# Kernel tuning notes

Hardware: AMD Instinct MI355X
Metric: run time of the kernel (lower is better)

Reference implementation:

```python
import jax, jax.numpy as jnp
import numpy as np

NL, NK = 10000, 2000          # ligand / keypoint node counts
ELL, EKL = 320000, 160000     # lig->lig and kp->lig edge counts
IN, HID, OUT = 128, 128, 128  # in_size, hidden_size, out_size
FDIM = 2 * IN + 1             # edge MLP input: [h_src, h_dst, dij]


def silu(x):
    return x * jax.nn.sigmoid(x)


def setup_inputs() -> dict:
    keys = iter(jax.random.split(jax.random.key(0), 64))

    def nrm(shape, scale=0.02):
        return jax.random.normal(next(keys), shape, dtype=jnp.float32) * scale

    d = {}
    d["h_lig"] = jax.random.normal(next(keys), (NL, IN), dtype=jnp.float32)
    d["h_kp"] = jax.random.normal(next(keys), (NK, IN), dtype=jnp.float32)
    d["x_lig"] = jax.random.normal(next(keys), (NL, 3), dtype=jnp.float32)
    d["x_kp"] = jax.random.normal(next(keys), (NK, 3), dtype=jnp.float32)
    # per-node normalizer (e.g. neighbor count); keep >= 1 to avoid blowup
    d["z_lig"] = jax.random.uniform(next(keys), (NL, 1), dtype=jnp.float32, minval=1.0, maxval=32.0)
    for e in ("ll", "kl"):
        d[e + "_eW1"] = nrm((FDIM, HID)); d[e + "_eb1"] = jnp.zeros((HID,), jnp.float32)
        d[e + "_eW2"] = nrm((HID, HID)); d[e + "_eb2"] = jnp.zeros((HID,), jnp.float32)
        d[e + "_aW"] = nrm((HID, 1)); d[e + "_ab"] = jnp.zeros((1,), jnp.float32)
        d[e + "_cW1"] = nrm((FDIM, HID)); d[e + "_cb1"] = jnp.zeros((HID,), jnp.float32)
        d[e + "_cW2"] = nrm((HID, HID)); d[e + "_cb2"] = jnp.zeros((HID,), jnp.float32)
        d[e + "_cW3"] = nrm((HID, 1), scale=0.001)  # xavier gain=0.001 final coord layer
    d["n_W1"] = nrm((IN + HID, HID)); d["n_b1"] = jnp.zeros((HID,), jnp.float32)
    d["n_W2"] = nrm((HID, OUT)); d["n_b2"] = jnp.zeros((OUT,), jnp.float32)
    d["ll_src"] = jax.random.randint(next(keys), (ELL,), 0, NL, dtype=jnp.int32)
    d["ll_dst"] = jax.random.randint(next(keys), (ELL,), 0, NL, dtype=jnp.int32)
    d["kl_src"] = jax.random.randint(next(keys), (EKL,), 0, NK, dtype=jnp.int32)
    d["kl_dst"] = jax.random.randint(next(keys), (EKL,), 0, NL, dtype=jnp.int32)
    return d


def _edge_messages(hs, hd, xs, xd, eW1, eb1, eW2, eb2, aW, ab, cW1, cb1, cW2, cb2, cW3):
    x_diff = xs - xd                                     # fn.u_sub_v
    dij = jnp.linalg.norm(x_diff, axis=1, keepdims=True)  # [E,1]
    x_diff = x_diff / (dij + 1.0)
    f = jnp.concatenate([hs, hd, dij], axis=1)           # [E, 2*IN+1]
    m = silu(f @ eW1 + eb1)
    m = silu(m @ eW2 + eb2)
    msg_h = m * jax.nn.sigmoid(m @ aW + ab)              # soft attention gate
    c = silu(f @ cW1 + cb1)
    c = silu(c @ cW2 + cb2)
    msg_x = (c @ cW3) * x_diff                           # use_tanh=False path
    return msg_h, msg_x


def reference(h_lig, h_kp, x_lig, x_kp, z_lig,
              ll_eW1, ll_eb1, ll_eW2, ll_eb2, ll_aW, ll_ab,
              ll_cW1, ll_cb1, ll_cW2, ll_cb2, ll_cW3,
              kl_eW1, kl_eb1, kl_eW2, kl_eb2, kl_aW, kl_ab,
              kl_cW1, kl_cb1, kl_cW2, kl_cb2, kl_cW3,
              n_W1, n_b1, n_W2, n_b2,
              ll_src, ll_dst, kl_src, kl_dst):
    # lig -> lig edges
    mh_ll, mx_ll = _edge_messages(h_lig[ll_src], h_lig[ll_dst], x_lig[ll_src], x_lig[ll_dst],
                                  ll_eW1, ll_eb1, ll_eW2, ll_eb2, ll_aW, ll_ab,
                                  ll_cW1, ll_cb1, ll_cW2, ll_cb2, ll_cW3)
    # kp -> lig edges
    mh_kl, mx_kl = _edge_messages(h_kp[kl_src], h_lig[kl_dst], x_kp[kl_src], x_lig[kl_dst],
                                  kl_eW1, kl_eb1, kl_eW2, kl_eb2, kl_aW, kl_ab,
                                  kl_cW1, kl_cb1, kl_cW2, kl_cb2, kl_cW3)
    nl = h_lig.shape[0]
    # multi_update_all with cross_reducer='sum', then per-node normalization by z
    h_neigh = (jax.ops.segment_sum(mh_ll, ll_dst, num_segments=nl)
               + jax.ops.segment_sum(mh_kl, kl_dst, num_segments=nl)) / z_lig
    x_neigh = (jax.ops.segment_sum(mx_ll, ll_dst, num_segments=nl)
               + jax.ops.segment_sum(mx_kl, kl_dst, num_segments=nl)) / z_lig
    nin = jnp.concatenate([h_lig, h_neigh], axis=1)
    h_out = h_lig + (silu(nin @ n_W1 + n_b1) @ n_W2 + n_b2)  # norm=False -> Identity
    x_out = x_lig + x_neigh
    return (h_out, x_out)
```

## Files before the change

### kernel.cpp

```cpp
#include <hip/hip_runtime.h>
#include <math.h>

#define EPB  32
#define MSTR 136
#define FSTR 264

typedef __attribute__((ext_vector_type(8))) short short8;
typedef __attribute__((ext_vector_type(4))) float f32x4;

__device__ __forceinline__ unsigned short f2bf(float x) {
    unsigned int u = __float_as_uint(x);
    u += 0x7fffu + ((u >> 16) & 1u);
    return (unsigned short)(u >> 16);
}
__device__ __forceinline__ float bf2f(short v) {
    return __uint_as_float(((unsigned int)(unsigned short)v) << 16);
}
__device__ __forceinline__ float fsilu(float x) {
    return x * (1.0f / (1.0f + __expf(-x)));
}
__device__ __forceinline__ float fsigm(float x) {
    return 1.0f / (1.0f + __expf(-x));
}
__device__ __forceinline__ void atomAddF(float* p, float v) {
    unsafeAtomicAdd(p, v);
}

struct PrepArgs { const float* src[10]; };

__global__ __launch_bounds__(256) void prep_hist_kernel(PrepArgs pa, short* __restrict__ wsb,
                                                        const int* __restrict__ lld,
                                                        const int* __restrict__ kld,
                                                        int* __restrict__ hist) {
    int idx = blockIdx.x * 256 + threadIdx.x;
    if (idx < 245760) {
        int pair = idx / 49152;
        int rem  = idx - pair * 49152;
        int second = (rem >= 32768) ? 1 : 0;
        int mi = pair * 2 + second;
        int within = second ? (rem - 32768) : rem;
        int n, k, K;
        if (second) { K = 128; n = within >> 7; k = within & 127; }
        else        { K = 256; n = within >> 8; k = within & 255; }
        int dstoff = pair * 49152 + second * 32768;
        wsb[dstoff + n * K + k] = (short)f2bf(pa.src[mi][k * 128 + n]);
        return;
    }
    idx -= 245760;
    if (idx < 320000) { atomicAdd(&hist[lld[idx]], 1); return; }
    idx -= 320000;
    if (idx < 160000) atomicAdd(&hist[10000 + kld[idx]], 1);
}

__global__ __launch_bounds__(256) void scan_kernel(const int* __restrict__ hist,
                                                   int* __restrict__ cursor) {
    __shared__ int bins[10000];
    __shared__ int ps[256];
    const int b = blockIdx.x, t = threadIdx.x;
    const int* h = hist + b * 10000;
    int* cur = cursor + b * 10000;
    for (int i = t; i < 10000; i += 256) bins[i] = h[i];
    __syncthreads();
    const int base = t * 40;
    int s = 0;
#pragma unroll 8
    for (int i = 0; i < 40; i++) { int ii = base + i; if (ii < 10000) s += bins[ii]; }
    ps[t] = s;
    __syncthreads();
    for (int off = 1; off < 256; off <<= 1) {
        int v = (t >= off) ? ps[t - off] : 0;
        __syncthreads();
        ps[t] += v;
        __syncthreads();
    }
    int run = ps[t] - s;
    for (int i = 0; i < 40; i++) {
        int ii = base + i;
        if (ii < 10000) { int c = bins[ii]; bins[ii] = run; run += c; }
    }
    __syncthreads();
    for (int i = t; i < 10000; i += 256) cur[i] = bins[i];
}

struct ProjDesc { const float* A; const short* Bt; short* out; const float* bias;
                  int rows; int ktb; int co; int hasb; };
struct CArgs {
    const int *lls, *lld, *kls, *kld;
    int* cursor;
    int *ll_ssrc, *ll_sdst, *kl_ssrc, *kl_sdst;
    ProjDesc d[8];
};

__global__ __launch_bounds__(256) void scatter_proj_kernel(CArgs ca) {
    __shared__ __align__(16) short a_lds[64 * MSTR];
    const int t = threadIdx.x;
    if (blockIdx.x < 1875) {
        int i = blockIdx.x * 256 + t;
        if (i < 320000) {
            int d = ca.lld[i];
            int p = atomicAdd(&ca.cursor[d], 1);
            ca.ll_ssrc[p] = ca.lls[i]; ca.ll_sdst[p] = d;
        } else if (i < 480000) {
            int j = i - 320000;
            int d = ca.kld[j];
            int p = atomicAdd(&ca.cursor[10000 + d], 1);
            ca.kl_ssrc[p] = ca.kls[j]; ca.kl_sdst[p] = d;
        }
        return;
    }
    const int pb = blockIdx.x - 1875;
    const int di = pb / 157, tile = pb - di * 157;
    const ProjDesc pd = ca.d[di];
    if (tile * 64 >= pd.rows) return;
    {
        const int r = t >> 2, q = t & 3;
        const int node = tile * 64 + r;
        short* arow = a_lds + r * MSTR + q * 32;
        if (node < pd.rows) {
            const float* ap = pd.A + (size_t)node * 128 + q * 32;
#pragma unroll
            for (int i = 0; i < 4; i++) {
                float4 v0 = *(const float4*)(ap + i * 8);
                float4 v1 = *(const float4*)(ap + i * 8 + 4);
                short8 o;
                o[0] = (short)f2bf(v0.x); o[1] = (short)f2bf(v0.y);
                o[2] = (short)f2bf(v0.z); o[3] = (short)f2bf(v0.w);
                o[4] = (short)f2bf(v1.x); o[5] = (short)f2bf(v1.y);
                o[6] = (short)f2bf(v1.z); o[7] = (short)f2bf(v1.w);
                *(short8*)(arow + i * 8) = o;
            }
        } else {
            short8 z = {0, 0, 0, 0, 0, 0, 0, 0};
#pragma unroll
            for (int i = 0; i < 4; i++) *(short8*)(arow + i * 8) = z;
        }
    }
    __syncthreads();

    const int ln = t & 63, wv = t >> 6;
    const int lrow = ln & 15, quad = ln >> 4;
    const int c0 = wv * 32 + lrow, c1 = c0 + 16;

    short8 bf0[4], bf1[4];
#pragma unroll
    for (int kt = 0; kt < 4; kt++) {
        bf0[kt] = *(const short8*)(pd.Bt + c0 * 256 + (pd.ktb + kt) * 32 + quad * 8);
        bf1[kt] = *(const short8*)(pd.Bt + c1 * 256 + (pd.ktb + kt) * 32 + quad * 8);
    }
    const float bb0 = pd.hasb ? pd.bias[c0] : 0.0f;
    const float bb1 = pd.hasb ? pd.bias[c1] : 0.0f;
#pragma unroll
    for (int mt = 0; mt < 4; mt++) {
        short8 af[4];
#pragma unroll
        for (int kt = 0; kt < 4; kt++)
            af[kt] = *(const short8*)(&a_lds[(mt * 16 + lrow) * MSTR + kt * 32 + quad * 8]);
        f32x4 a0 = {0.f, 0.f, 0.f, 0.f}, a1 = {0.f, 0.f, 0.f, 0.f};
#pragma unroll
        for (int kt = 0; kt < 4; kt++) {
            a0 = __builtin_amdgcn_mfma_f32_16x16x32_bf16(af[kt], bf0[kt], a0, 0, 0, 0);
            a1 = __builtin_amdgcn_mfma_f32_16x16x32_bf16(af[kt], bf1[kt], a1, 0, 0, 0);
        }
#pragma unroll
        for (int r = 0; r < 4; r++) {
            const int node = tile * 64 + mt * 16 + quad * 4 + r;
            if (node < pd.rows) {
                pd.out[(size_t)node * 256 + pd.co + c0] = (short)f2bf(a0[r] + bb0);
                pd.out[(size_t)node * 256 + pd.co + c1] = (short)f2bf(a1[r] + bb1);
            }
        }
    }
}

struct EdgeSet {
    const short *Ps, *Pd;
    const float *xs, *xd;
    const int *esrc, *edst;
    const float *w256e, *w256c;
    const short *W2t, *cW2t;
    const float *b2e, *b2c;
    const float *aW, *ab, *cW3;
};
struct EdgePair { EdgeSet s[2]; int split; };

__global__ __launch_bounds__(256, 8) void edge_kernel(EdgePair ep,
                                                      float* __restrict__ hne,
                                                      float* __restrict__ xne)
{
    __shared__ __align__(16) char mbuf[EPB * MSTR * 4];
    __shared__ float sv_l[EPB];
    __shared__ float gate_l[EPB];
    __shared__ float xdf[3][EPB];
    __shared__ int   dstl[EPB];
    __shared__ float gp[4][EPB];

    short* mh = (short*)mbuf;
    short* mc = (short*)(mbuf + EPB * MSTR * 2);
    float* msg = (float*)mbuf;

    const int isKL = (blockIdx.x >= ep.split) ? 1 : 0;
    const EdgeSet P = ep.s[isKL];
    const int eb = (blockIdx.x - (isKL ? ep.split : 0)) * EPB;
    const int t = threadIdx.x;

    {
        const int e = t >> 3, q = t & 7;
        const int eid = eb + e;
        const int s = P.esrc[eid], d = P.edst[eid];
        float dx = P.xs[s * 3 + 0] - P.xd[d * 3 + 0];
        float dy = P.xs[s * 3 + 1] - P.xd[d * 3 + 1];
        float dz = P.xs[s * 3 + 2] - P.xd[d * 3 + 2];
        float dd = sqrtf(dx * dx + dy * dy + dz * dz);
        if (q == 0) {
            dstl[e] = d;
            float inv = 1.0f / (dd + 1.0f);
            xdf[0][e] = dx * inv; xdf[1][e] = dy * inv; xdf[2][e] = dz * inv;
        }
        const short* psrow = P.Ps + (size_t)s * 256 + q * 16;
        const short* pdrow = P.Pd + (size_t)d * 256 + q * 16;
#pragma unroll
        for (int path = 0; path < 2; path++) {
            const short* ps = psrow + path * 128;
            const short* pq = pdrow + path * 128;
            const float* wq = (path ? P.w256c : P.w256e) + q * 16;
            short* mrow = (path ? mc : mh) + e * MSTR + q * 16;
#pragma unroll
            for (int i = 0; i < 2; i++) {
                short8 a = *(const short8*)(ps + i * 8);
                short8 b = *(const short8*)(pq + i * 8);
                float4 wA = *(const float4*)(wq + i * 8);
                float4 wB = *(const float4*)(wq + i * 8 + 4);
                short8 o;
                o[0] = (short)f2bf(fsilu(bf2f(a[0]) + bf2f(b[0]) + dd * wA.x));
                o[1] = (short)f2bf(fsilu(bf2f(a[1]) + bf2f(b[1]) + dd * wA.y));
                o[2] = (short)f2bf(fsilu(bf2f(a[2]) + bf2f(b[2]) + dd * wA.z));
                o[3] = (short)f2bf(fsilu(bf2f(a[3]) + bf2f(b[3]) + dd * wA.w));
                o[4] = (short)f2bf(fsilu(bf2f(a[4]) + bf2f(b[4]) + dd * wB.x));
                o[5] = (short)f2bf(fsilu(bf2f(a[5]) + bf2f(b[5]) + dd * wB.y));
                o[6] = (short)f2bf(fsilu(bf2f(a[6]) + bf2f(b[6]) + dd * wB.z));
                o[7] = (short)f2bf(fsilu(bf2f(a[7]) + bf2f(b[7]) + dd * wB.w));
                *(short8*)(mrow + i * 8) = o;
            }
        }
    }
    __syncthreads();

    const int ln = t & 63, wv = t >> 6;
    const int lrow = ln & 15, quad = ln >> 4;
    const int c0 = wv * 32 + lrow, c1 = c0 + 16;

    {
        short8 bf0[4], bf1[4];
#pragma unroll
        for (int kt = 0; kt < 4; kt++) {
            bf0[kt] = *(const short8*)(P.cW2t + c0 * 128 + kt * 32 + quad * 8);
            bf1[kt] = *(const short8*)(P.cW2t + c1 * 128 + kt * 32 + quad * 8);
        }
        const float cw0 = P.cW3[c0], cw1 = P.cW3[c1];
        const float bb0 = P.b2c[c0], bb1 = P.b2c[c1];
#pragma unroll
        for (int mt = 0; mt < 2; mt++) {
            short8 af[4];
#pragma unroll
            for (int kt = 0; kt < 4; kt++)
                af[kt] = *(const short8*)(&mc[(mt * 16 + lrow) * MSTR + kt * 32 + quad * 8]);
            f32x4 a0 = {0.f, 0.f, 0.f, 0.f}, a1 = {0.f, 0.f, 0.f, 0.f};
#pragma unroll
            for (int kt = 0; kt < 4; kt++) {
                a0 = __builtin_amdgcn_mfma_f32_16x16x32_bf16(af[kt], bf0[kt], a0, 0, 0, 0);
                a1 = __builtin_amdgcn_mfma_f32_16x16x32_bf16(af[kt], bf1[kt], a1, 0, 0, 0);
            }
#pragma unroll
            for (int r = 0; r < 4; r++) {
                float v0 = fsilu(a0[r] + bb0);
                float v1 = fsilu(a1[r] + bb1);
                float g = v0 * cw0 + v1 * cw1;
                g += __shfl_xor(g, 1, 64);
                g += __shfl_xor(g, 2, 64);
                g += __shfl_xor(g, 4, 64);
                g += __shfl_xor(g, 8, 64);
                if (lrow == 0) gp[wv][mt * 16 + quad * 4 + r] = g;
            }
        }
    }
    __syncthreads();
    if (t < EPB) sv_l[t] = gp[0][t] + gp[1][t] + gp[2][t] + gp[3][t];
    __syncthreads();

    float m2s[2][8];
    {
        short8 bf0[4], bf1[4];
#pragma unroll
        for (int kt = 0; kt < 4; kt++) {
            bf0[kt] = *(const short8*)(P.W2t + c0 * 128 + kt * 32 + quad * 8);
            bf1[kt] = *(const short8*)(P.W2t + c1 * 128 + kt * 32 + quad * 8);
        }
        const float aw0 = P.aW[c0], aw1 = P.aW[c1];
        const float bb0 = P.b2e[c0], bb1 = P.b2e[c1];
#pragma unroll
        for (int mt = 0; mt < 2; mt++) {
            short8 af[4];
#pragma unroll
            for (int kt = 0; kt < 4; kt++)
                af[kt] = *(const short8*)(&mh[(mt * 16 + lrow) * MSTR + kt * 32 + quad * 8]);
            f32x4 a0 = {0.f, 0.f, 0.f, 0.f}, a1 = {0.f, 0.f, 0.f, 0.f};
#pragma unroll
            for (int kt = 0; kt < 4; kt++) {
                a0 = __builtin_amdgcn_mfma_f32_16x16x32_bf16(af[kt], bf0[kt], a0, 0, 0, 0);
                a1 = __builtin_amdgcn_mfma_f32_16x16x32_bf16(af[kt], bf1[kt], a1, 0, 0, 0);
            }
#pragma unroll
            for (int r = 0; r < 4; r++) {
                float v0 = fsilu(a0[r] + bb0);
                float v1 = fsilu(a1[r] + bb1);
                m2s[mt][r] = v0; m2s[mt][4 + r] = v1;
                float g = v0 * aw0 + v1 * aw1;
                g += __shfl_xor(g, 1, 64);
                g += __shfl_xor(g, 2, 64);
                g += __shfl_xor(g, 4, 64);
                g += __shfl_xor(g, 8, 64);
                if (lrow == 0) gp[wv][mt * 16 + quad * 4 + r] = g;
            }
        }
    }
    __syncthreads();
    if (t < EPB) gate_l[t] = fsigm(gp[0][t] + gp[1][t] + gp[2][t] + gp[3][t] + P.ab[0]);
#pragma unroll
    for (int mt = 0; mt < 2; mt++)
#pragma unroll
        for (int r = 0; r < 4; r++) {
            const int erow = mt * 16 + quad * 4 + r;
            msg[erow * 132 + c0] = m2s[mt][r];
            msg[erow * 132 + c1] = m2s[mt][4 + r];
        }
    __syncthreads();

    if (t < 128) {
        const int col = t;
        float acc = 0.0f;
        int cur = dstl[0];
#pragma unroll 4
        for (int e = 0; e < EPB; e++) {
            const int d = dstl[e];
            if (d != cur) {
                atomAddF(&hne[(size_t)cur * 128 + col], acc);
                acc = 0.0f; cur = d;
            }
            acc += msg[e * 132 + col] * gate_l[e];
        }
        atomAddF(&hne[(size_t)cur * 128 + col], acc);
    } else if (t < 131) {
        const int ax = t - 128;
        float acc = 0.0f;
        int cur = dstl[0];
        for (int e = 0; e < EPB; e++) {
            const int d = dstl[e];
            if (d != cur) {
                atomAddF(&xne[cur * 3 + ax], acc);
                acc = 0.0f; cur = d;
            }
            acc += sv_l[e] * xdf[ax][e];
        }
        atomAddF(&xne[cur * 3 + ax], acc);
    }
}

__global__ __launch_bounds__(256) void node_kernel(
    const float* __restrict__ h_lig, const float* __restrict__ zlig,
    const short* __restrict__ W1t, const float* __restrict__ b1v,
    const short* __restrict__ W2t, const float* __restrict__ b2v,
    const float* __restrict__ x_lig,
    float* __restrict__ acc_h, float* __restrict__ acc_x)
{
    __shared__ __align__(16) short f_lds[64 * FSTR];
    __shared__ __align__(16) short m_lds[64 * MSTR];
    const int t = threadIdx.x;
    const int nb = blockIdx.x * 64;

    {
        const int e = t >> 2, q = t & 3;
        const int node = nb + e;
        short* frow = &f_lds[e * FSTR + q * 32];
        if (node < 10000) {
            const float zi = 1.0f / zlig[node];
            const float4* hp = (const float4*)(h_lig + (size_t)node * 128 + q * 32);
            const float4* np = (const float4*)(acc_h + (size_t)node * 128 + q * 32);
#pragma unroll
            for (int i = 0; i < 8; i++) {
                float4 v = hp[i];
                *(ushort4*)(frow + i * 4) =
                    make_ushort4(f2bf(v.x), f2bf(v.y), f2bf(v.z), f2bf(v.w));
            }
#pragma unroll
            for (int i = 0; i < 8; i++) {
                float4 v = np[i];
                *(ushort4*)(frow + 128 + i * 4) =
                    make_ushort4(f2bf(v.x * zi), f2bf(v.y * zi), f2bf(v.z * zi), f2bf(v.w * zi));
            }
        } else {
            const ushort4 zz = make_ushort4(0, 0, 0, 0);
#pragma unroll
            for (int i = 0; i < 8; i++) {
                *(ushort4*)(frow + i * 4) = zz;
                *(ushort4*)(frow + 128 + i * 4) = zz;
            }
        }
    }
    __syncthreads();

    const int ln = t & 63, wv = t >> 6;
    const int lrow = ln & 15, quad = ln >> 4;
    const int c0 = wv * 32 + lrow, c1 = c0 + 16;

    {
        short8 bf0[8], bf1[8];
#pragma unroll
// ... 66 lines not shown
}

extern "C" void kernel_launch(void* const* d_in, const int* in_sizes, int n_in,
                              void* d_out, int out_size, void* d_ws, size_t ws_size,
                              hipStream_t stream)
{
    (void)in_sizes; (void)n_in; (void)ws_size;
    const float* h_lig  = (const float*)d_in[0];
    const float* h_kp   = (const float*)d_in[1];
    const float* x_lig  = (const float*)d_in[2];
    const float* x_kp   = (const float*)d_in[3];
    const float* z_lig  = (const float*)d_in[4];
    const float* ll_eW1 = (const float*)d_in[5];
    const float* ll_eb1 = (const float*)d_in[6];
    const float* ll_eW2 = (const float*)d_in[7];
    const float* ll_eb2 = (const float*)d_in[8];
    const float* ll_aW  = (const float*)d_in[9];
    const float* ll_ab  = (const float*)d_in[10];
    const float* ll_cW1 = (const float*)d_in[11];
    const float* ll_cb1 = (const float*)d_in[12];
    const float* ll_cW2 = (const float*)d_in[13];
    const float* ll_cb2 = (const float*)d_in[14];
    const float* ll_cW3 = (const float*)d_in[15];
    const float* kl_eW1 = (const float*)d_in[16];
    const float* kl_eb1 = (const float*)d_in[17];
    const float* kl_eW2 = (const float*)d_in[18];
    const float* kl_eb2 = (const float*)d_in[19];
    const float* kl_aW  = (const float*)d_in[20];
    const float* kl_ab  = (const float*)d_in[21];
    const float* kl_cW1 = (const float*)d_in[22];
    const float* kl_cb1 = (const float*)d_in[23];
    const float* kl_cW2 = (const float*)d_in[24];
    const float* kl_cb2 = (const float*)d_in[25];
    const float* kl_cW3 = (const float*)d_in[26];
    const float* n_W1   = (const float*)d_in[27];
    const float* n_b1   = (const float*)d_in[28];
    const float* n_W2   = (const float*)d_in[29];
    const float* n_b2   = (const float*)d_in[30];
    const int* ll_src = (const int*)d_in[31];
    const int* ll_dst = (const int*)d_in[32];
    const int* kl_src = (const int*)d_in[33];
    const int* kl_dst = (const int*)d_in[34];

    float* out = (float*)d_out;
    float* hne = out;
    float* xne = out + 1280000;

    char* wsc = (char*)d_ws;
    short* wsb    = (short*)wsc;
    short* P_ll_s = (short*)(wsc +   491520);
    short* P_ll_d = (short*)(wsc +  5611520);
    short* P_kl_s = (short*)(wsc + 10731520);
    short* P_kl_d = (short*)(wsc + 11755520);
    int* ll_ssrc  = (int*)(wsc + 16875520);
    int* ll_sdst  = (int*)(wsc + 18155520);
    int* kl_ssrc  = (int*)(wsc + 19435520);
    int* kl_sdst  = (int*)(wsc + 20075520);
    int* hist     = (int*)(wsc + 20715520);
    int* cursor   = (int*)(wsc + 20795520);

    hipMemsetAsync(d_out, 0, (size_t)out_size * sizeof(float), stream);
    hipMemsetAsync(hist, 0, 80000, stream);

    {
        PrepArgs pa;
        pa.src[0] = ll_eW1; pa.src[1] = ll_eW2; pa.src[2] = ll_cW1; pa.src[3] = ll_cW2;
        pa.src[4] = kl_eW1; pa.src[5] = kl_eW2; pa.src[6] = kl_cW1; pa.src[7] = kl_cW2;
        pa.src[8] = n_W1;   pa.src[9] = n_W2;
        prep_hist_kernel<<<2835, 256, 0, stream>>>(pa, wsb, ll_dst, kl_dst, hist);
    }
    scan_kernel<<<2, 256, 0, stream>>>(hist, cursor);
    {
        CArgs ca;
        ca.lls = ll_src; ca.lld = ll_dst; ca.kls = kl_src; ca.kld = kl_dst;
        ca.cursor = cursor;
        ca.ll_ssrc = ll_ssrc; ca.ll_sdst = ll_sdst;
        ca.kl_ssrc = kl_ssrc; ca.kl_sdst = kl_sdst;
        ca.d[0] = { h_lig, wsb + 0,      P_ll_s, ll_eb1, 10000, 0, 0,   0 };
        ca.d[1] = { h_lig, wsb + 49152,  P_ll_s, ll_cb1, 10000, 0, 128, 0 };
        ca.d[2] = { h_lig, wsb + 0,      P_ll_d, ll_eb1, 10000, 4, 0,   1 };
        ca.d[3] = { h_lig, wsb + 49152,  P_ll_d, ll_cb1, 10000, 4, 128, 1 };
        ca.d[4] = { h_kp,  wsb + 98304,  P_kl_s, kl_eb1,  2000, 0, 0,   0 };
        ca.d[5] = { h_kp,  wsb + 147456, P_kl_s, kl_cb1,  2000, 0, 128, 0 };
        ca.d[6] = { h_lig, wsb + 98304,  P_kl_d, kl_eb1, 10000, 4, 0,   1 };
        ca.d[7] = { h_lig, wsb + 147456, P_kl_d, kl_cb1, 10000, 4, 128, 1 };
        scatter_proj_kernel<<<1875 + 8 * 157, 256, 0, stream>>>(ca);
    }
    {
        EdgePair ep;
        ep.split = 10000;
        ep.s[0] = { P_ll_s, P_ll_d, x_lig, x_lig, ll_ssrc, ll_sdst,
                    ll_eW1 + 256 * 128, ll_cW1 + 256 * 128,
                    wsb + 32768, wsb + 81920, ll_eb2, ll_cb2,
                    ll_aW, ll_ab, ll_cW3 };
        ep.s[1] = { P_kl_s, P_kl_d, x_kp, x_lig, kl_ssrc, kl_sdst,
                    kl_eW1 + 256 * 128, kl_cW1 + 256 * 128,
                    wsb + 131072, wsb + 180224, kl_eb2, kl_cb2,
                    kl_aW, kl_ab, kl_cW3 };
        edge_kernel<<<15000, 256, 0, stream>>>(ep, hne, xne);
    }
    node_kernel<<<157, 256, 0, stream>>>(
        h_lig, z_lig, wsb + 196608, n_b1, wsb + 229376, n_b2,
        x_lig, hne, xne);
}
```

Measured before the change: 412.5 us.

## Make edge kernel wave-independent with register-resident MFMA and merge scan into projection

The edge kernel is restructured so each 64-lane wave owns 16 edges and computes the full 128-column output in registers. This removes the shared-memory staging, block-wide barriers and serial per-column segment reduction. Scatter-add uses a shuffle reduction when all 16 edges share a destination, otherwise per-lane atomics. The separate scan kernel is folded into the projection kernel, and the edge-sorting scatter becomes its own launch. The cost is that each wave reloads the full W2 weights from global or cache, uses more registers, and issues more atomics when destinations differ.

```diff
diff --git a/kernel.cpp b/kernel.cpp
--- a/kernel.cpp
+++ b/kernel.cpp
@@ -1,7 +1,6 @@
 #include <hip/hip_runtime.h>
 #include <math.h>
 
-#define EPB  32
 #define MSTR 136
 #define FSTR 264
 
@@ -52,65 +51,49 @@
     if (idx < 160000) atomicAdd(&hist[10000 + kld[idx]], 1);
 }
 
-__global__ __launch_bounds__(256) void scan_kernel(const int* __restrict__ hist,
-                                                   int* __restrict__ cursor) {
-    __shared__ int bins[10000];
-    __shared__ int ps[256];
-    const int b = blockIdx.x, t = threadIdx.x;
-    const int* h = hist + b * 10000;
-    int* cur = cursor + b * 10000;
-    for (int i = t; i < 10000; i += 256) bins[i] = h[i];
-    __syncthreads();
-    const int base = t * 40;
-    int s = 0;
-#pragma unroll 8
-    for (int i = 0; i < 40; i++) { int ii = base + i; if (ii < 10000) s += bins[ii]; }
-    ps[t] = s;
-    __syncthreads();
-    for (int off = 1; off < 256; off <<= 1) {
-        int v = (t >= off) ? ps[t - off] : 0;
-        __syncthreads();
-        ps[t] += v;
-        __syncthreads();
-    }
-    int run = ps[t] - s;
-    for (int i = 0; i < 40; i++) {
-        int ii = base + i;
-        if (ii < 10000) { int c = bins[ii]; bins[ii] = run; run += c; }
-    }
-    __syncthreads();
-    for (int i = t; i < 10000; i += 256) cur[i] = bins[i];
-}
-
 struct ProjDesc { const float* A; const short* Bt; short* out; const float* bias;
                   int rows; int ktb; int co; int hasb; };
-struct CArgs {
-    const int *lls, *lld, *kls, *kld;
-    int* cursor;
-    int *ll_ssrc, *ll_sdst, *kl_ssrc, *kl_sdst;
+struct SPArgs {
+    const int* hist; int* cursor;
     ProjDesc d[8];
 };
 
-__global__ __launch_bounds__(256) void scatter_proj_kernel(CArgs ca) {
-    __shared__ __align__(16) short a_lds[64 * MSTR];
+__global__ __launch_bounds__(256) void scan_proj_kernel(SPArgs sp) {
+    __shared__ __align__(16) char smem[41024];
     const int t = threadIdx.x;
-    if (blockIdx.x < 1875) {
-        int i = blockIdx.x * 256 + t;
-        if (i < 320000) {
-            int d = ca.lld[i];
-            int p = atomicAdd(&ca.cursor[d], 1);
-            ca.ll_ssrc[p] = ca.lls[i]; ca.ll_sdst[p] = d;
-        } else if (i < 480000) {
-            int j = i - 320000;
-            int d = ca.kld[j];
-            int p = atomicAdd(&ca.cursor[10000 + d], 1);
-            ca.kl_ssrc[p] = ca.kls[j]; ca.kl_sdst[p] = d;
-        }
+    if (blockIdx.x < 2) {
+        int* bins = (int*)smem;
+        int* ps   = (int*)(smem + 40000);
+        const int b = blockIdx.x;
+        const int* h = sp.hist + b * 10000;
+        int* cur = sp.cursor + b * 10000;
+        for (int i = t; i < 10000; i += 256) bins[i] = h[i];
+        __syncthreads();
+        const int base = t * 40;
+        int s = 0;
+#pragma unroll 8
+        for (int i = 0; i < 40; i++) { int ii = base + i; if (ii < 10000) s += bins[ii]; }
+        ps[t] = s;
+        __syncthreads();
+        for (int off = 1; off < 256; off <<= 1) {
+            int v = (t >= off) ? ps[t - off] : 0;
+            __syncthreads();
+            ps[t] += v;
+            __syncthreads();
+        }
+        int run = ps[t] - s;
+        for (int i = 0; i < 40; i++) {
+            int ii = base + i;
+            if (ii < 10000) { int c = bins[ii]; bins[ii] = run; run += c; }
+        }
+        __syncthreads();
+        for (int i = t; i < 10000; i += 256) cur[i] = bins[i];
         return;
     }
-    const int pb = blockIdx.x - 1875;
+    short* a_lds = (short*)smem;
+    const int pb = blockIdx.x - 2;
     const int di = pb / 157, tile = pb - di * 157;
-    const ProjDesc pd = ca.d[di];
+    const ProjDesc pd = sp.d[di];
     if (tile * 64 >= pd.rows) return;
     {
         const int r = t >> 2, q = t & 3;
@@ -172,6 +155,26 @@
     }
 }
 
+__global__ __launch_bounds__(256) void scatter_kernel(const int* __restrict__ lls,
+                                                      const int* __restrict__ lld,
+                                                      const int* __restrict__ kls,
+                                                      const int* __restrict__ kld,
+                                                      int* __restrict__ cursor,
+                                                      int* __restrict__ ll_ssrc, int* __restrict__ ll_sdst,
+                                                      int* __restrict__ kl_ssrc, int* __restrict__ kl_sdst) {
+    int i = blockIdx.x * 256 + threadIdx.x;
+    if (i < 320000) {
+        int d = lld[i];
+        int p = atomicAdd(&cursor[d], 1);
+        ll_ssrc[p] = lls[i]; ll_sdst[p] = d;
+    } else if (i < 480000) {
+        int j = i - 320000;
+        int d = kld[j];
+        int p = atomicAdd(&cursor[10000 + d], 1);
+        kl_ssrc[p] = kls[j]; kl_sdst[p] = d;
+    }
+}
+
 struct EdgeSet {
     const short *Ps, *Pd;
     const float *xs, *xd;
@@ -181,187 +184,197 @@
     const float *b2e, *b2c;
     const float *aW, *ab, *cW3;
 };
-struct EdgePair { EdgeSet s[2]; int split; };
-
-__global__ __launch_bounds__(256, 8) void edge_kernel(EdgePair ep,
-                                                      float* __restrict__ hne,
-                                                      float* __restrict__ xne)
+struct EdgePair { EdgeSet s[2]; int llwaves; };
+
+__global__ __launch_bounds__(256) void edge_kernel(EdgePair ep,
+                                                   float* __restrict__ hne,
+                                                   float* __restrict__ xne)
 {
-    __shared__ __align__(16) char mbuf[EPB * MSTR * 4];
-    __shared__ float sv_l[EPB];
-    __shared__ float gate_l[EPB];
-    __shared__ float xdf[3][EPB];
-    __shared__ int   dstl[EPB];
-    __shared__ float gp[4][EPB];
-
-    short* mh = (short*)mbuf;
-    short* mc = (short*)(mbuf + EPB * MSTR * 2);
-    float* msg = (float*)mbuf;
-
-    const int isKL = (blockIdx.x >= ep.split) ? 1 : 0;
+    const int t = threadIdx.x;
+    const int wv = t >> 6, ln = t & 63;
+    const int lrow = ln & 15, quad = ln >> 4;
+    const int gw = blockIdx.x * 4 + wv;
+    const int isKL = (gw >= ep.llwaves) ? 1 : 0;
     const EdgeSet P = ep.s[isKL];
-    const int eb = (blockIdx.x - (isKL ? ep.split : 0)) * EPB;
-    const int t = threadIdx.x;
-
-    {
-        const int e = t >> 3, q = t & 7;
-        const int eid = eb + e;
-        const int s = P.esrc[eid], d = P.edst[eid];
-        float dx = P.xs[s * 3 + 0] - P.xd[d * 3 + 0];
-        float dy = P.xs[s * 3 + 1] - P.xd[d * 3 + 1];
-        float dz = P.xs[s * 3 + 2] - P.xd[d * 3 + 2];
-        float dd = sqrtf(dx * dx + dy * dy + dz * dz);
-        if (q == 0) {
-            dstl[e] = d;
-            float inv = 1.0f / (dd + 1.0f);
-            xdf[0][e] = dx * inv; xdf[1][e] = dy * inv; xdf[2][e] = dz * inv;
-        }
-        const short* psrow = P.Ps + (size_t)s * 256 + q * 16;
-        const short* pdrow = P.Pd + (size_t)d * 256 + q * 16;
-#pragma unroll
-        for (int path = 0; path < 2; path++) {
-            const short* ps = psrow + path * 128;
-            const short* pq = pdrow + path * 128;
-            const float* wq = (path ? P.w256c : P.w256e) + q * 16;
-            short* mrow = (path ? mc : mh) + e * MSTR + q * 16;
-#pragma unroll
-            for (int i = 0; i < 2; i++) {
-                short8 a = *(const short8*)(ps + i * 8);
-                short8 b = *(const short8*)(pq + i * 8);
-                float4 wA = *(const float4*)(wq + i * 8);
-                float4 wB = *(const float4*)(wq + i * 8 + 4);
-                short8 o;
-                o[0] = (short)f2bf(fsilu(bf2f(a[0]) + bf2f(b[0]) + dd * wA.x));
-                o[1] = (short)f2bf(fsilu(bf2f(a[1]) + bf2f(b[1]) + dd * wA.y));
-                o[2] = (short)f2bf(fsilu(bf2f(a[2]) + bf2f(b[2]) + dd * wA.z));
-                o[3] = (short)f2bf(fsilu(bf2f(a[3]) + bf2f(b[3]) + dd * wA.w));
-                o[4] = (short)f2bf(fsilu(bf2f(a[4]) + bf2f(b[4]) + dd * wB.x));
-                o[5] = (short)f2bf(fsilu(bf2f(a[5]) + bf2f(b[5]) + dd * wB.y));
-                o[6] = (short)f2bf(fsilu(bf2f(a[6]) + bf2f(b[6]) + dd * wB.z));
-                o[7] = (short)f2bf(fsilu(bf2f(a[7]) + bf2f(b[7]) + dd * wB.w));
-                *(short8*)(mrow + i * 8) = o;
-            }
-        }
-    }
-    __syncthreads();
-
-    const int ln = t & 63, wv = t >> 6;
-    const int lrow = ln & 15, quad = ln >> 4;
-    const int c0 = wv * 32 + lrow, c1 = c0 + 16;
-
-    {
-        short8 bf0[4], bf1[4];
+    const int ew = (isKL ? gw - ep.llwaves : gw) * 16;
+
+    const int me = ew + lrow;
+    const int s = P.esrc[me], d = P.edst[me];
+    const float dx = P.xs[s * 3 + 0] - P.xd[d * 3 + 0];
+    const float dy = P.xs[s * 3 + 1] - P.xd[d * 3 + 1];
+    const float dz = P.xs[s * 3 + 2] - P.xd[d * 3 + 2];
+    const float dd = sqrtf(dx * dx + dy * dy + dz * dz);
+    const float inv = 1.0f / (dd + 1.0f);
+    const float xdf0 = dx * inv, xdf1 = dy * inv, xdf2 = dz * inv;
+
+    const int dfirst = P.edst[ew], dlast = P.edst[ew + 15];
+    const bool uni = (dfirst == dlast);
+    int d_r[4];
+#pragma unroll
+    for (int r = 0; r < 4; r++) d_r[r] = P.edst[ew + quad * 4 + r];
+
+    const int kbase = quad * 8;
+
+    float sv0, sv1, sv2, sv3;
+    {
+        short8 af[4];
+        const short* ps = P.Ps + (size_t)s * 256 + 128;
+        const short* pq = P.Pd + (size_t)d * 256 + 128;
 #pragma unroll
         for (int kt = 0; kt < 4; kt++) {
-            bf0[kt] = *(const short8*)(P.cW2t + c0 * 128 + kt * 32 + quad * 8);
-            bf1[kt] = *(const short8*)(P.cW2t + c1 * 128 + kt * 32 + quad * 8);
-        }
-        const float cw0 = P.cW3[c0], cw1 = P.cW3[c1];
-        const float bb0 = P.b2c[c0], bb1 = P.b2c[c1];
-#pragma unroll
-        for (int mt = 0; mt < 2; mt++) {
-            short8 af[4];
+            const int k = kt * 32 + kbase;
+            short8 a = *(const short8*)(ps + k);
+            short8 b = *(const short8*)(pq + k);
+            float4 wA = *(const float4*)(P.w256c + k);
+            float4 wB = *(const float4*)(P.w256c + k + 4);
+            short8 o;
+            o[0] = (short)f2bf(fsilu(bf2f(a[0]) + bf2f(b[0]) + dd * wA.x));
+            o[1] = (short)f2bf(fsilu(bf2f(a[1]) + bf2f(b[1]) + dd * wA.y));
+            o[2] = (short)f2bf(fsilu(bf2f(a[2]) + bf2f(b[2]) + dd * wA.z));
+            o[3] = (short)f2bf(fsilu(bf2f(a[3]) + bf2f(b[3]) + dd * wA.w));
+            o[4] = (short)f2bf(fsilu(bf2f(a[4]) + bf2f(b[4]) + dd * wB.x));
+            o[5] = (short)f2bf(fsilu(bf2f(a[5]) + bf2f(b[5]) + dd * wB.y));
+            o[6] = (short)f2bf(fsilu(bf2f(a[6]) + bf2f(b[6]) + dd * wB.z));
+            o[7] = (short)f2bf(fsilu(bf2f(a[7]) + bf2f(b[7]) + dd * wB.w));
+            af[kt] = o;
+        }
+        float gp0 = 0.f, gp1 = 0.f, gp2 = 0.f, gp3 = 0.f;
+#pragma unroll
+        for (int n = 0; n < 8; n++) {
+            const int col = n * 16 + lrow;
+            short8 bf[4];
 #pragma unroll
             for (int kt = 0; kt < 4; kt++)
-                af[kt] = *(const short8*)(&mc[(mt * 16 + lrow) * MSTR + kt * 32 + quad * 8]);
-            f32x4 a0 = {0.f, 0.f, 0.f, 0.f}, a1 = {0.f, 0.f, 0.f, 0.f};
-#pragma unroll
-            for (int kt = 0; kt < 4; kt++) {
-                a0 = __builtin_amdgcn_mfma_f32_16x16x32_bf16(af[kt], bf0[kt], a0, 0, 0, 0);
-                a1 = __builtin_amdgcn_mfma_f32_16x16x32_bf16(af[kt], bf1[kt], a1, 0, 0, 0);
-            }
+                bf[kt] = *(const short8*)(P.cW2t + col * 128 + kt * 32 + kbase);
+            f32x4 acc = {0.f, 0.f, 0.f, 0.f};
+#pragma unroll
+            for (int kt = 0; kt < 4; kt++)
+                acc = __builtin_amdgcn_mfma_f32_16x16x32_bf16(af[kt], bf[kt], acc, 0, 0, 0);
+            const float bb = P.b2c[col], w3 = P.cW3[col];
+            gp0 += fsilu(acc[0] + bb) * w3;
+            gp1 += fsilu(acc[1] + bb) * w3;
+            gp2 += fsilu(acc[2] + bb) * w3;
+            gp3 += fsilu(acc[3] + bb) * w3;
+        }
+#pragma unroll
+        for (int m = 1; m < 16; m <<= 1) {
+            gp0 += __shfl_xor(gp0, m, 64);
+            gp1 += __shfl_xor(gp1, m, 64);
+            gp2 += __shfl_xor(gp2, m, 64);
+            gp3 += __shfl_xor(gp3, m, 64);
+        }
+        sv0 = gp0; sv1 = gp1; sv2 = gp2; sv3 = gp3;
+    }
+    {
+        const int srcl = (lrow >> 2) * 16;
+        float s0 = __shfl(sv0, srcl, 64), s1 = __shfl(sv1, srcl, 64);
+        float s2 = __shfl(sv2, srcl, 64), s3 = __shfl(sv3, srcl, 64);
+        const int j = lrow & 3;
+        const float sve = (j == 0) ? s0 : ((j == 1) ? s1 : ((j == 2) ? s2 : s3));
+        float vx0 = sve * xdf0, vx1 = sve * xdf1, vx2 = sve * xdf2;
+        if (uni) {
+#pragma unroll
+            for (int m = 1; m < 16; m <<= 1) {
+                vx0 += __shfl_xor(vx0, m, 64);
+                vx1 += __shfl_xor(vx1, m, 64);
+                vx2 += __shfl_xor(vx2, m, 64);
+            }
+            if (ln == 0) {
+                atomAddF(&xne[dfirst * 3 + 0], vx0);
+                atomAddF(&xne[dfirst * 3 + 1], vx1);
+                atomAddF(&xne[dfirst * 3 + 2], vx2);
+            }
+        } else if (ln < 16) {
+            atomAddF(&xne[d * 3 + 0], vx0);
+            atomAddF(&xne[d * 3 + 1], vx1);
+            atomAddF(&xne[d * 3 + 2], vx2);
+        }
+    }
+
+    {
+        short8 af[4];
+        const short* ps = P.Ps + (size_t)s * 256;
+        const short* pq = P.Pd + (size_t)d * 256;
+#pragma unroll
+        for (int kt = 0; kt < 4; kt++) {
+            const int k = kt * 32 + kbase;
+            short8 a = *(const short8*)(ps + k);
+            short8 b = *(const short8*)(pq + k);
+            float4 wA = *(const float4*)(P.w256e + k);
+            float4 wB = *(const float4*)(P.w256e + k + 4);
+            short8 o;
+            o[0] = (short)f2bf(fsilu(bf2f(a[0]) + bf2f(b[0]) + dd * wA.x));
+            o[1] = (short)f2bf(fsilu(bf2f(a[1]) + bf2f(b[1]) + dd * wA.y));
+            o[2] = (short)f2bf(fsilu(bf2f(a[2]) + bf2f(b[2]) + dd * wA.z));
+            o[3] = (short)f2bf(fsilu(bf2f(a[3]) + bf2f(b[3]) + dd * wA.w));
+            o[4] = (short)f2bf(fsilu(bf2f(a[4]) + bf2f(b[4]) + dd * wB.x));
+            o[5] = (short)f2bf(fsilu(bf2f(a[5]) + bf2f(b[5]) + dd * wB.y));
+            o[6] = (short)f2bf(fsilu(bf2f(a[6]) + bf2f(b[6]) + dd * wB.z));
+            o[7] = (short)f2bf(fsilu(bf2f(a[7]) + bf2f(b[7]) + dd * wB.w));
+            af[kt] = o;
+        }
+        float m2[8][4];
+        float gp0 = 0.f, gp1 = 0.f, gp2 = 0.f, gp3 = 0.f;
+#pragma unroll
+        for (int n = 0; n < 8; n++) {
+            const int col = n * 16 + lrow;
+            short8 bf[4];
+#pragma unroll
+            for (int kt = 0; kt < 4; kt++)
+                bf[kt] = *(const short8*)(P.W2t + col * 128 + kt * 32 + kbase);
+            f32x4 acc = {0.f, 0.f, 0.f, 0.f};
+#pragma unroll
+            for (int kt = 0; kt < 4; kt++)
+                acc = __builtin_amdgcn_mfma_f32_16x16x32_bf16(af[kt], bf[kt], acc, 0, 0, 0);
+            const float bb = P.b2e[col], aw = P.aW[col];
 #pragma unroll
             for (int r = 0; r < 4; r++) {
-                float v0 = fsilu(a0[r] + bb0);
-                float v1 = fsilu(a1[r] + bb1);
-                float g = v0 * cw0 + v1 * cw1;
-                g += __shfl_xor(g, 1, 64);
-                g += __shfl_xor(g, 2, 64);
-                g += __shfl_xor(g, 4, 64);
-                g += __shfl_xor(g, 8, 64);
-                if (lrow == 0) gp[wv][mt * 16 + quad * 4 + r] = g;
-            }
-        }
-    }
-    __syncthreads();
-    if (t < EPB) sv_l[t] = gp[0][t] + gp[1][t] + gp[2][t] + gp[3][t];
-    __syncthreads();
-
-    float m2s[2][8];
-    {
-        short8 bf0[4], bf1[4];
-#pragma unroll
-        for (int kt = 0; kt < 4; kt++) {
-            bf0[kt] = *(const short8*)(P.W2t + c0 * 128 + kt * 32 + quad * 8);
-            bf1[kt] = *(const short8*)(P.W2t + c1 * 128 + kt * 32 + quad * 8);
-        }
-        const float aw0 = P.aW[c0], aw1 = P.aW[c1];
-        const float bb0 = P.b2e[c0], bb1 = P.b2e[c1];
-#pragma unroll
-        for (int mt = 0; mt < 2; mt++) {
-            short8 af[4];
-#pragma unroll
-            for (int kt = 0; kt < 4; kt++)
-                af[kt] = *(const short8*)(&mh[(mt * 16 + lrow) * MSTR + kt * 32 + quad * 8]);
-            f32x4 a0 = {0.f, 0.f, 0.f, 0.f}, a1 = {0.f, 0.f, 0.f, 0.f};
-#pragma unroll
-            for (int kt = 0; kt < 4; kt++) {
-                a0 = __builtin_amdgcn_mfma_f32_16x16x32_bf16(af[kt], bf0[kt], a0, 0, 0, 0);
-                a1 = __builtin_amdgcn_mfma_f32_16x16x32_bf16(af[kt], bf1[kt], a1, 0, 0, 0);
-            }
-#pragma unroll
-            for (int r = 0; r < 4; r++) {
-                float v0 = fsilu(a0[r] + bb0);
-                float v1 = fsilu(a1[r] + bb1);
-                m2s[mt][r] = v0; m2s[mt][4 + r] = v1;
-                float g = v0 * aw0 + v1 * aw1;
-                g += __shfl_xor(g, 1, 64);
-                g += __shfl_xor(g, 2, 64);
-                g += __shfl_xor(g, 4, 64);
-                g += __shfl_xor(g, 8, 64);
-                if (lrow == 0) gp[wv][mt * 16 + quad * 4 + r] = g;
-            }
-        }
-    }
-    __syncthreads();
-    if (t < EPB) gate_l[t] = fsigm(gp[0][t] + gp[1][t] + gp[2][t] + gp[3][t] + P.ab[0]);
-#pragma unroll
-    for (int mt = 0; mt < 2; mt++)
-#pragma unroll
-        for (int r = 0; r < 4; r++) {
-            const int erow = mt * 16 + quad * 4 + r;
-            msg[erow * 132 + c0] = m2s[mt][r];
-            msg[erow * 132 + c1] = m2s[mt][4 + r];
-        }
-    __syncthreads();
-
-    if (t < 128) {
-        const int col = t;
-        float acc = 0.0f;
-        int cur = dstl[0];
-#pragma unroll 4
-        for (int e = 0; e < EPB; e++) {
-            const int d = dstl[e];
-            if (d != cur) {
-                atomAddF(&hne[(size_t)cur * 128 + col], acc);
-                acc = 0.0f; cur = d;
-            }
-            acc += msg[e * 132 + col] * gate_l[e];
-        }
-        atomAddF(&hne[(size_t)cur * 128 + col], acc);
-    } else if (t < 131) {
-        const int ax = t - 128;
-        float acc = 0.0f;
-        int cur = dstl[0];
-        for (int e = 0; e < EPB; e++) {
-            const int d = dstl[e];
-            if (d != cur) {
-                atomAddF(&xne[cur * 3 + ax], acc);
-                acc = 0.0f; cur = d;
-            }
-            acc += sv_l[e] * xdf[ax][e];
-        }
-        atomAddF(&xne[cur * 3 + ax], acc);
+                float v = fsilu(acc[r] + bb);
+                m2[n][r] = v;
+            }
+            gp0 += m2[n][0] * aw; gp1 += m2[n][1] * aw;
+            gp2 += m2[n][2] * aw; gp3 += m2[n][3] * aw;
+        }
+        const float abv = P.ab[0];
+#pragma unroll
+        for (int m = 1; m < 16; m <<= 1) {
+            gp0 += __shfl_xor(gp0, m, 64);
+            gp1 += __shfl_xor(gp1, m, 64);
+            gp2 += __shfl_xor(gp2, m, 64);
+            gp3 += __shfl_xor(gp3, m, 64);
+        }
+        float gate[4];
+        gate[0] = fsigm(gp0 + abv); gate[1] = fsigm(gp1 + abv);
+        gate[2] = fsigm(gp2 + abv); gate[3] = fsigm(gp3 + abv);
+
+        if (uni) {
+            const size_t drow = (size_t)dfirst * 128;
+#pragma unroll
+            for (int n = 0; n < 8; n++) {
+                float ssum = m2[n][0] * gate[0] + m2[n][1] * gate[1]
+                           + m2[n][2] * gate[2] + m2[n][3] * gate[3];
+                ssum += __shfl_xor(ssum, 16, 64);
+                ssum += __shfl_xor(ssum, 32, 64);
+                if (quad == 0) atomAddF(&hne[drow + n * 16 + lrow], ssum);
+            }
+        } else {
+#pragma unroll
+            for (int n = 0; n < 8; n++) {
+                const int col = n * 16 + lrow;
+                int cur = d_r[0];
+                float acc2 = m2[n][0] * gate[0];
+#pragma unroll
+                for (int r = 1; r < 4; r++) {
+                    float v = m2[n][r] * gate[r];
+                    if (d_r[r] == cur) acc2 += v;
+                    else {
+                        atomAddF(&hne[(size_t)cur * 128 + col], acc2);
+                        cur = d_r[r]; acc2 = v;
+                    }
+                }
+                atomAddF(&hne[(size_t)cur * 128 + col], acc2);
+            }
+        }
     }
 }
 
@@ -551,26 +564,24 @@
         pa.src[8] = n_W1;   pa.src[9] = n_W2;
         prep_hist_kernel<<<2835, 256, 0, stream>>>(pa, wsb, ll_dst, kl_dst, hist);
     }
-    scan_kernel<<<2, 256, 0, stream>>>(hist, cursor);
-    {
-        CArgs ca;
-        ca.lls = ll_src; ca.lld = ll_dst; ca.kls = kl_src; ca.kld = kl_dst;
-        ca.cursor = cursor;
-        ca.ll_ssrc = ll_ssrc; ca.ll_sdst = ll_sdst;
-        ca.kl_ssrc = kl_ssrc; ca.kl_sdst = kl_sdst;
-        ca.d[0] = { h_lig, wsb + 0,      P_ll_s, ll_eb1, 10000, 0, 0,   0 };
-        ca.d[1] = { h_lig, wsb + 49152,  P_ll_s, ll_cb1, 10000, 0, 128, 0 };
-        ca.d[2] = { h_lig, wsb + 0,      P_ll_d, ll_eb1, 10000, 4, 0,   1 };
-        ca.d[3] = { h_lig, wsb + 49152,  P_ll_d, ll_cb1, 10000, 4, 128, 1 };
-        ca.d[4] = { h_kp,  wsb + 98304,  P_kl_s, kl_eb1,  2000, 0, 0,   0 };
-        ca.d[5] = { h_kp,  wsb + 147456, P_kl_s, kl_cb1,  2000, 0, 128, 0 };
-        ca.d[6] = { h_lig, wsb + 98304,  P_kl_d, kl_eb1, 10000, 4, 0,   1 };
-        ca.d[7] = { h_lig, wsb + 147456, P_kl_d, kl_cb1, 10000, 4, 128, 1 };
-        scatter_proj_kernel<<<1875 + 8 * 157, 256, 0, stream>>>(ca);
-    }
+    {
+        SPArgs sp;
+        sp.hist = hist; sp.cursor = cursor;
+        sp.d[0] = { h_lig, wsb + 0,      P_ll_s, ll_eb1, 10000, 0, 0,   0 };
+        sp.d[1] = { h_lig, wsb + 49152,  P_ll_s, ll_cb1, 10000, 0, 128, 0 };
+        sp.d[2] = { h_lig, wsb + 0,      P_ll_d, ll_eb1, 10000, 4, 0,   1 };
+        sp.d[3] = { h_lig, wsb + 49152,  P_ll_d, ll_cb1, 10000, 4, 128, 1 };
+        sp.d[4] = { h_kp,  wsb + 98304,  P_kl_s, kl_eb1,  2000, 0, 0,   0 };
+        sp.d[5] = { h_kp,  wsb + 147456, P_kl_s, kl_cb1,  2000, 0, 128, 0 };
+        sp.d[6] = { h_lig, wsb + 98304,  P_kl_d, kl_eb1, 10000, 4, 0,   1 };
+        sp.d[7] = { h_lig, wsb + 147456, P_kl_d, kl_cb1, 10000, 4, 128, 1 };
+        scan_proj_kernel<<<2 + 8 * 157, 256, 0, stream>>>(sp);
+    }
+    scatter_kernel<<<1875, 256, 0, stream>>>(ll_src, ll_dst, kl_src, kl_dst, cursor,
+                                             ll_ssrc, ll_sdst, kl_ssrc, kl_sdst);
     {
         EdgePair ep;
-        ep.split = 10000;
+        ep.llwaves = 20000;
         ep.s[0] = { P_ll_s, P_ll_d, x_lig, x_lig, ll_ssrc, ll_sdst,
                     ll_eW1 + 256 * 128, ll_cW1 + 256 * 128,
                     wsb + 32768, wsb + 81920, ll_eb2, ll_cb2,
@@ -579,7 +590,7 @@
                     kl_eW1 + 256 * 128, kl_cW1 + 256 * 128,
                     wsb + 131072, wsb + 180224, kl_eb2, kl_cb2,
                     kl_aW, kl_ab, kl_cW3 };
-        edge_kernel<<<15000, 256, 0, stream>>>(ep, hne, xne);
+        edge_kernel<<<7500, 256, 0, stream>>>(ep, hne, xne);
     }
     node_kernel<<<157, 256, 0, stream>>>(
         h_lig, z_lig, wsb + 196608, n_b1, wsb + 229376, n_b2,
```

Result: slower. 559.4 us (+35.6%).

## Merge scan into projection kernel, pack edge indices, drop a barrier

Applied to the files above, without the earlier changes.

The standalone two-block scan kernel is folded into the projection kernel as two extra blocks. The scatter moves into its own kernel after the projections, so the scan's serial work overlaps with the projection GEMMs instead of being launched alone. Sorted source and destination indices are packed into int2 so each edge's indices load in one access. In the edge kernel, the coord-path and gate-path partial sums go to separate shared arrays, which removes one __syncthreads pair. The scan now reads the histogram directly from global memory instead of staging it in LDS, and one kernel launch is added back.

```diff
diff --git a/kernel.cpp b/kernel.cpp
--- a/kernel.cpp
+++ b/kernel.cpp
@@ -52,65 +52,43 @@
     if (idx < 160000) atomicAdd(&hist[10000 + kld[idx]], 1);
 }
 
-__global__ __launch_bounds__(256) void scan_kernel(const int* __restrict__ hist,
-                                                   int* __restrict__ cursor) {
-    __shared__ int bins[10000];
-    __shared__ int ps[256];
-    const int b = blockIdx.x, t = threadIdx.x;
-    const int* h = hist + b * 10000;
-    int* cur = cursor + b * 10000;
-    for (int i = t; i < 10000; i += 256) bins[i] = h[i];
-    __syncthreads();
-    const int base = t * 40;
-    int s = 0;
-#pragma unroll 8
-    for (int i = 0; i < 40; i++) { int ii = base + i; if (ii < 10000) s += bins[ii]; }
-    ps[t] = s;
-    __syncthreads();
-    for (int off = 1; off < 256; off <<= 1) {
-        int v = (t >= off) ? ps[t - off] : 0;
-        __syncthreads();
-        ps[t] += v;
-        __syncthreads();
-    }
-    int run = ps[t] - s;
-    for (int i = 0; i < 40; i++) {
-        int ii = base + i;
-        if (ii < 10000) { int c = bins[ii]; bins[ii] = run; run += c; }
-    }
-    __syncthreads();
-    for (int i = t; i < 10000; i += 256) cur[i] = bins[i];
-}
-
 struct ProjDesc { const float* A; const short* Bt; short* out; const float* bias;
                   int rows; int ktb; int co; int hasb; };
-struct CArgs {
-    const int *lls, *lld, *kls, *kld;
-    int* cursor;
-    int *ll_ssrc, *ll_sdst, *kl_ssrc, *kl_sdst;
+struct SPArgs {
+    const int* hist; int* cursor;
     ProjDesc d[8];
 };
 
-__global__ __launch_bounds__(256) void scatter_proj_kernel(CArgs ca) {
+__global__ __launch_bounds__(256) void scan_proj_kernel(SPArgs sp) {
     __shared__ __align__(16) short a_lds[64 * MSTR];
+    __shared__ int ps[256];
     const int t = threadIdx.x;
-    if (blockIdx.x < 1875) {
-        int i = blockIdx.x * 256 + t;
-        if (i < 320000) {
-            int d = ca.lld[i];
-            int p = atomicAdd(&ca.cursor[d], 1);
-            ca.ll_ssrc[p] = ca.lls[i]; ca.ll_sdst[p] = d;
-        } else if (i < 480000) {
-            int j = i - 320000;
-            int d = ca.kld[j];
-            int p = atomicAdd(&ca.cursor[10000 + d], 1);
-            ca.kl_ssrc[p] = ca.kls[j]; ca.kl_sdst[p] = d;
+    if (blockIdx.x < 2) {
+        const int b = blockIdx.x;
+        const int* h = sp.hist + b * 10000;
+        int* cur = sp.cursor + b * 10000;
+        const int base = t * 40;
+        int s = 0;
+#pragma unroll 8
+        for (int i = 0; i < 40; i++) { int ii = base + i; if (ii < 10000) s += h[ii]; }
+        ps[t] = s;
+        __syncthreads();
+        for (int off = 1; off < 256; off <<= 1) {
+            int v = (t >= off) ? ps[t - off] : 0;
+            __syncthreads();
+            ps[t] += v;
+            __syncthreads();
+        }
+        int run = ps[t] - s;
+        for (int i = 0; i < 40; i++) {
+            int ii = base + i;
+            if (ii < 10000) { cur[ii] = run; run += h[ii]; }
         }
         return;
     }
-    const int pb = blockIdx.x - 1875;
+    const int pb = blockIdx.x - 2;
     const int di = pb / 157, tile = pb - di * 157;
-    const ProjDesc pd = ca.d[di];
+    const ProjDesc pd = sp.d[di];
     if (tile * 64 >= pd.rows) return;
     {
         const int r = t >> 2, q = t & 3;
@@ -172,10 +150,30 @@
     }
 }
 
+__global__ __launch_bounds__(256) void scatter_kernel(const int* __restrict__ lls,
+                                                      const int* __restrict__ lld,
+                                                      const int* __restrict__ kls,
+                                                      const int* __restrict__ kld,
+                                                      int* __restrict__ cursor,
+                                                      int2* __restrict__ ll_sdp,
+                                                      int2* __restrict__ kl_sdp) {
+    int i = blockIdx.x * 256 + threadIdx.x;
+    if (i < 320000) {
+        int d = lld[i];
+        int p = atomicAdd(&cursor[d], 1);
+        ll_sdp[p] = make_int2(lls[i], d);
+    } else if (i < 480000) {
+        int j = i - 320000;
+        int d = kld[j];
+        int p = atomicAdd(&cursor[10000 + d], 1);
+        kl_sdp[p] = make_int2(kls[j], d);
+    }
+}
+
 struct EdgeSet {
     const short *Ps, *Pd;
     const float *xs, *xd;
-    const int *esrc, *edst;
+    const int2 *esd;
     const float *w256e, *w256c;
     const short *W2t, *cW2t;
     const float *b2e, *b2c;
@@ -192,7 +190,8 @@
     __shared__ float gate_l[EPB];
     __shared__ float xdf[3][EPB];
     __shared__ int   dstl[EPB];
-    __shared__ float gp[4][EPB];
+    __shared__ float gpc[4][EPB];
+    __shared__ float gpe[4][EPB];
 
     short* mh = (short*)mbuf;
     short* mc = (short*)(mbuf + EPB * MSTR * 2);
@@ -206,7 +205,8 @@
     {
         const int e = t >> 3, q = t & 7;
         const int eid = eb + e;
-        const int s = P.esrc[eid], d = P.edst[eid];
+        const int2 sd = P.esd[eid];
+        const int s = sd.x, d = sd.y;
         float dx = P.xs[s * 3 + 0] - P.xd[d * 3 + 0];
         float dy = P.xs[s * 3 + 1] - P.xd[d * 3 + 1];
         float dz = P.xs[s * 3 + 2] - P.xd[d * 3 + 2];
@@ -279,13 +279,10 @@
                 g += __shfl_xor(g, 2, 64);
                 g += __shfl_xor(g, 4, 64);
                 g += __shfl_xor(g, 8, 64);
-                if (lrow == 0) gp[wv][mt * 16 + quad * 4 + r] = g;
-            }
-        }
-    }
-    __syncthreads();
-    if (t < EPB) sv_l[t] = gp[0][t] + gp[1][t] + gp[2][t] + gp[3][t];
-    __syncthreads();
+                if (lrow == 0) gpc[wv][mt * 16 + quad * 4 + r] = g;
+            }
+        }
+    }
 
     float m2s[2][8];
     {
@@ -319,12 +316,16 @@
                 g += __shfl_xor(g, 2, 64);
                 g += __shfl_xor(g, 4, 64);
                 g += __shfl_xor(g, 8, 64);
-                if (lrow == 0) gp[wv][mt * 16 + quad * 4 + r] = g;
+                if (lrow == 0) gpe[wv][mt * 16 + quad * 4 + r] = g;
             }
         }
     }
     __syncthreads();
-    if (t < EPB) gate_l[t] = fsigm(gp[0][t] + gp[1][t] + gp[2][t] + gp[3][t] + P.ab[0]);
+
+    if (t < EPB) {
+        sv_l[t]   = gpc[0][t] + gpc[1][t] + gpc[2][t] + gpc[3][t];
+        gate_l[t] = fsigm(gpe[0][t] + gpe[1][t] + gpe[2][t] + gpe[3][t] + P.ab[0]);
+    }
 #pragma unroll
     for (int mt = 0; mt < 2; mt++)
 #pragma unroll
@@ -534,10 +535,8 @@
     short* P_ll_d = (short*)(wsc +  5611520);
     short* P_kl_s = (short*)(wsc + 10731520);
     short* P_kl_d = (short*)(wsc + 11755520);
-    int* ll_ssrc  = (int*)(wsc + 16875520);
-    int* ll_sdst  = (int*)(wsc + 18155520);
-    int* kl_ssrc  = (int*)(wsc + 19435520);
-    int* kl_sdst  = (int*)(wsc + 20075520);
+    int2* ll_sdp  = (int2*)(wsc + 16875520);
+    int2* kl_sdp  = (int2*)(wsc + 19435520);
     int* hist     = (int*)(wsc + 20715520);
     int* cursor   = (int*)(wsc + 20795520);
 
@@ -551,31 +550,29 @@
         pa.src[8] = n_W1;   pa.src[9] = n_W2;
         prep_hist_kernel<<<2835, 256, 0, stream>>>(pa, wsb, ll_dst, kl_dst, hist);
     }
-    scan_kernel<<<2, 256, 0, stream>>>(hist, cursor);
-    {
-        CArgs ca;
-        ca.lls = ll_src; ca.lld = ll_dst; ca.kls = kl_src; ca.kld = kl_dst;
-        ca.cursor = cursor;
-        ca.ll_ssrc = ll_ssrc; ca.ll_sdst = ll_sdst;
-        ca.kl_ssrc = kl_ssrc; ca.kl_sdst = kl_sdst;
-        ca.d[0] = { h_lig, wsb + 0,      P_ll_s, ll_eb1, 10000, 0, 0,   0 };
-        ca.d[1] = { h_lig, wsb + 49152,  P_ll_s, ll_cb1, 10000, 0, 128, 0 };
-        ca.d[2] = { h_lig, wsb + 0,      P_ll_d, ll_eb1, 10000, 4, 0,   1 };
-        ca.d[3] = { h_lig, wsb + 49152,  P_ll_d, ll_cb1, 10000, 4, 128, 1 };
-        ca.d[4] = { h_kp,  wsb + 98304,  P_kl_s, kl_eb1,  2000, 0, 0,   0 };
-        ca.d[5] = { h_kp,  wsb + 147456, P_kl_s, kl_cb1,  2000, 0, 128, 0 };
-        ca.d[6] = { h_lig, wsb + 98304,  P_kl_d, kl_eb1, 10000, 4, 0,   1 };
-        ca.d[7] = { h_lig, wsb + 147456, P_kl_d, kl_cb1, 10000, 4, 128, 1 };
-        scatter_proj_kernel<<<1875 + 8 * 157, 256, 0, stream>>>(ca);
-    }
+    {
+        SPArgs sp;
+        sp.hist = hist; sp.cursor = cursor;
+        sp.d[0] = { h_lig, wsb + 0,      P_ll_s, ll_eb1, 10000, 0, 0,   0 };
+        sp.d[1] = { h_lig, wsb + 49152,  P_ll_s, ll_cb1, 10000, 0, 128, 0 };
+        sp.d[2] = { h_lig, wsb + 0,      P_ll_d, ll_eb1, 10000, 4, 0,   1 };
+        sp.d[3] = { h_lig, wsb + 49152,  P_ll_d, ll_cb1, 10000, 4, 128, 1 };
+        sp.d[4] = { h_kp,  wsb + 98304,  P_kl_s, kl_eb1,  2000, 0, 0,   0 };
+        sp.d[5] = { h_kp,  wsb + 147456, P_kl_s, kl_cb1,  2000, 0, 128, 0 };
+        sp.d[6] = { h_lig, wsb + 98304,  P_kl_d, kl_eb1, 10000, 4, 0,   1 };
+        sp.d[7] = { h_lig, wsb + 147456, P_kl_d, kl_cb1, 10000, 4, 128, 1 };
+        scan_proj_kernel<<<2 + 8 * 157, 256, 0, stream>>>(sp);
+    }
+    scatter_kernel<<<1875, 256, 0, stream>>>(ll_src, ll_dst, kl_src, kl_dst, cursor,
+                                             ll_sdp, kl_sdp);
     {
         EdgePair ep;
         ep.split = 10000;
-        ep.s[0] = { P_ll_s, P_ll_d, x_lig, x_lig, ll_ssrc, ll_sdst,
+        ep.s[0] = { P_ll_s, P_ll_d, x_lig, x_lig, ll_sdp,
                     ll_eW1 + 256 * 128, ll_cW1 + 256 * 128,
                     wsb + 32768, wsb + 81920, ll_eb2, ll_cb2,
                     ll_aW, ll_ab, ll_cW3 };
-        ep.s[1] = { P_kl_s, P_kl_d, x_kp, x_lig, kl_ssrc, kl_sdst,
+        ep.s[1] = { P_kl_s, P_kl_d, x_kp, x_lig, kl_sdp,
                     kl_eW1 + 256 * 128, kl_cW1 + 256 * 128,
                     wsb + 131072, wsb + 180224, kl_eb2, kl_cb2,
                     kl_aW, kl_ab, kl_cW3 };
```

Measured after the change: 427.4 us. 1.04x slower.
